# Kernel optimization log

Measured on AMD Instinct MI355X. Metric: run time of the kernel, lower is better.

## Reference

```python
import jax, jax.numpy as jnp
import numpy as np

# Dimensions: state [N, d, n, 2] with last axis = (q, p)
N, D, NN = 256, 8, 32
FEAT = D * NN          # flattened q features = 256
HID = 256              # MLP hidden width
DT = 0.01              # integration step
STEPS = 100            # number of RK4 steps (sequential)


def setup_inputs() -> dict:
    key = jax.random.key(0)
    k0, k1, k2 = jax.random.split(key, 3)
    x0 = 0.1 * jax.random.normal(k0, (N, D, NN, 2), dtype=jnp.float32)
    W1 = jax.random.normal(k1, (FEAT, HID), dtype=jnp.float32) / np.float32(np.sqrt(FEAT))
    b1 = jnp.zeros((HID,), dtype=jnp.float32)
    W2 = jax.random.normal(k2, (HID, 1), dtype=jnp.float32) / np.float32(np.sqrt(HID))
    b2 = jnp.zeros((1,), dtype=jnp.float32)
    return {"x0": x0, "W1": W1, "b1": b1, "W2": W2, "b2": b2}


def _hamiltonian(x, W1, b1, W2, b2):
    # x: [N, d, n, 2] -> H: [N]
    q = x[..., 0]
    p = x[..., 1]
    kinetic = 0.5 * jnp.sum(p * p, axis=(1, 2))          # [N]
    qf = q.reshape(q.shape[0], -1)                        # [N, d*n]
    h = jnp.tanh(qf @ W1 + b1)                            # [N, HID]
    V = (h @ W2 + b2)[:, 0]                               # [N]
    return kinetic + V


def _vector_field(x, params):
    # Hamiltonian vector field: dq/dt = dH/dp, dp/dt = -dH/dq (t-independent)
    g = jax.grad(lambda xx: jnp.sum(_hamiltonian(xx, *params)))(x)  # [N,d,n,2]
    return jnp.stack([g[..., 1], -g[..., 0]], axis=-1)


def _rk4_step(x, eps, params):
    k1 = _vector_field(x, params)
    k2 = _vector_field(x + 0.5 * eps * k1, params)
    k3 = _vector_field(x + 0.5 * eps * k2, params)
    k4 = _vector_field(x + eps * k3, params)
    return x + (eps / 6.0) * (k1 + 2.0 * k2 + 2.0 * k3 + k4)


def reference(x0, W1, b1, W2, b2):
    params = (W1, b1, W2, b2)
    eps = jnp.float32(DT)

    def step(x, _):
        return _rk4_step(x, eps, params), None

    xT, _ = jax.lax.scan(step, x0, None, length=STEPS)
    return xT
```

## Files before the change

kernel.cpp:

```cpp
#include <hip/hip_runtime.h>
#include <stdint.h>


typedef _Float16 v8h __attribute__((ext_vector_type(8)));
typedef float v4f __attribute__((ext_vector_type(4)));

#define NSTEPS 100
#define NEX 25
#define WS 264
#define US 272

#define MFMA_AV(C, A, B) \
    asm("v_mfma_f32_16x16x32_f16 %0, %1, %2, %0" : "+v"(C) : "v"(A), "a"(B))

__device__ __forceinline__ float bfly4(float x) {
    float a = x, b = x;
    asm("v_permlane16_swap_b32 %0, %1" : "+v"(a), "+v"(b));
    float s = a + b;
    float c = s, d = s;
    asm("v_permlane32_swap_b32 %0, %1" : "+v"(c), "+v"(d));
    return c + d;
}

__device__ __forceinline__ float ueval2(float zz, float w4) {
    float e_ = __expf(zz);
    float r_ = __builtin_amdgcn_rcpf(e_ + 1.f);
    return w4 * __builtin_fmaf(-r_, r_, r_);
}

__global__ __launch_bounds__(1024, 4)
void ham_kernel(const float* __restrict__ x0, const float* __restrict__ W1,
                const float* __restrict__ b1, const float* __restrict__ W2,
                float* __restrict__ out)
{
    __shared__ __align__(16)  _Float16 wldsT[256 * WS];
    __shared__ __align__(128) char     upool[20480];
    float*    mscr = (float*)upool;
    _Float16* ubuf = (_Float16*)upool;

    const int t = threadIdx.x;
    const int w = t >> 6;
    const int l = t & 63;
    const int quad = l >> 4;
    const int s = l & 15;
    const int c0 = 16 * w + s;
    const int blk = blockIdx.x;
    const int sel = (s & 3) * US;

    {
        const int c = t & 255;
        const int rbase = (t >> 8) * 64;
        #pragma unroll 1
        for (int r0 = 0; r0 < 64; r0 += 8) {
            v8h h;
            #pragma unroll
            for (int j = 0; j < 8; ++j)
                h[j] = (_Float16)W1[(rbase + r0 + j) * 256 + c];
            *(v8h*)(wldsT + c * WS + rbase + r0) = h;
        }
    }
    __syncthreads();

    v8h wF0[8];
    #pragma unroll
    for (int kk = 0; kk < 8; ++kk)
        wF0[kk] = *(const v8h*)(wldsT + c0 * WS + 32 * kk + 8 * quad);

    v8h wM0[8];
    float* scr0 = mscr + w * 320;
    #pragma unroll
    for (int kb = 0; kb < 16; ++kb) {
        v8h aM[8];
        #pragma unroll
        for (int kk = 0; kk < 8; ++kk)
            aM[kk] = *(const v8h*)(wldsT + (16 * kb + s) * WS
                                          + 32 * kk + 8 * quad);
        v4f D0 = {0.f,0.f,0.f,0.f};
        #pragma unroll
        for (int kk = 0; kk < 8; ++kk)
            D0 = __builtin_amdgcn_mfma_f32_16x16x32_f16(aM[kk], wF0[kk], D0, 0, 0, 0);
        *(v4f*)(scr0 + s * 20 + 4 * quad) = D0;
        asm volatile("s_waitcnt lgkmcnt(0)" ::: "memory");
        if ((quad >> 1) == (kb & 1)) {
            #pragma unroll
            for (int j = 0; j < 8; ++j)
                wM0[kb >> 1][j] = (_Float16)scr0[s * 20 + 8 * (quad & 1) + j];
        }
        asm volatile("s_waitcnt lgkmcnt(0)" ::: "memory");
    }
    __syncthreads();

    const float b1r0 = b1[c0];
    const float w4 = 4.f * W2[c0];
    float2 qp0 = ((const float2*)(x0 + (size_t)blk * 512))[c0];
    const float q0o0 = qp0.x, p0o0 = qp0.y;

    if (quad == 0) {
        ubuf[c0] = (_Float16)q0o0;
        ubuf[US + c0] = (_Float16)p0o0;
        ubuf[2 * US + c0] = (_Float16)0.f;
        ubuf[3 * US + c0] = (_Float16)0.f;
    }
    __syncthreads();
    float z1, P;
    {
        const _Float16* ab = ubuf + sel + 8 * quad;
        v4f C0a = {0.f,0.f,0.f,0.f}, C0b = {0.f,0.f,0.f,0.f};
        #pragma unroll
        for (int kk = 0; kk < 8; kk += 2) {
            v8h a0 = *(const v8h*)(ab + 32 * kk);
            v8h a1 = *(const v8h*)(ab + 32 * (kk + 1));
            C0a = __builtin_amdgcn_mfma_f32_16x16x32_f16(a0, wF0[kk], C0a, 0, 0, 0);
            C0b = __builtin_amdgcn_mfma_f32_16x16x32_f16(a1, wF0[kk + 1], C0b, 0, 0, 0);
        }
        v4f C0s = C0a + C0b;
        z1 = C0s[0] + b1r0;  P = C0s[1];
    }
    __syncthreads();

    const float dt = 0.01f, hdt = 0.005f, dt6 = 0.01f / 6.f;
    const float dtdt6 = dt * dt6, hdt2 = hdt * hdt, dthdt = dt * hdt;
    const float fourdt = 4.f * dt;
    const float qf  = (float)quad;
    const float cPn   = -(qf * 0.25f * dt6);
    const float K2cz1 = 2.f * qf * dt;
    const float K2B   = qf * (4.f - qf) * dtdt6 * 0.25f;
    const float K2Vn  = -(qf * dtdt6 * 0.5f);
    const float K2hdt = 2.f * hdt;
    const float K2hdt2n = -2.f * hdt2;
    const float K2dt  = 2.f * dt;
    const float K2dthdtn = -2.f * dthdt;
    const float wB  = 3.f - qf;

    const int cw = c0 ^ (quad << 3);
    const int R0 = 4 * quad;
    const int wo0 = (R0 + 0) * US + cw;
    const int wo1 = (R0 + 1) * US + (cw ^ 32);
    const int wo2 = (R0 + 2) * US + cw;
    const int wo3 = (R0 + 3) * US + (cw ^ 32);
    const int sx = (s >> 2) & 3;
    const int rbase = s * US + 8 * (quad ^ sx);
    const int sodd = (s & 1) << 5;
    const _Float16* pe = ubuf + rbase + sodd;
    const _Float16* po = ubuf + rbase + 32 - sodd;

    float SBp = 0.f, SVp = 0.f;
    float Y1L = 0.f, Y2L = 0.f;
    float S1p = 0.f, S23p = 0.f;
    float cn = 99.f - qf;

    #pragma unroll 1
    for (int e = 0; e < NEX; ++e) {
        const int bo = (e & 1) * (16 * US);

        float Pp  = __builtin_fmaf(cPn, SBp, P);
        float zp2 = __builtin_fmaf(K2cz1, P, z1 + z1);
        zp2 = __builtin_fmaf(K2B, SBp, zp2);
        zp2 = __builtin_fmaf(K2Vn, SVp, zp2);
        float zb2 = __builtin_fmaf(K2hdt, Pp, zp2);
        float zc2 = __builtin_fmaf(K2hdt2n, Y1L, zb2);
        float zd2 = __builtin_fmaf(K2dt, Pp, zp2);
        zd2 = __builtin_fmaf(K2dthdtn, Y2L, zd2);

        float ua = ueval2(zp2, w4);
        float ub = ueval2(zb2, w4);
        float uc = ueval2(zc2, w4);
        float ud = ueval2(zd2, w4);

        ubuf[bo + wo0] = (_Float16)ua;
        ubuf[bo + wo1] = (_Float16)ub;
        ubuf[bo + wo2] = (_Float16)uc;
        ubuf[bo + wo3] = (_Float16)ud;
        __syncthreads();

        v4f C0s;
        {
            v4f C0a = {0.f,0.f,0.f,0.f}, C0b = {0.f,0.f,0.f,0.f};
            #pragma unroll
            for (int kk = 0; kk < 8; kk += 2) {
                v8h a0 = *(const v8h*)(pe + bo + 32 * kk);
                v8h a1 = *(const v8h*)(po + bo + 32 * kk);
                MFMA_AV(C0a, a0, wM0[kk]);
                MFMA_AV(C0b, a1, wM0[kk + 1]);
            }
            C0s = C0a + C0b;
        }

        float Y1 = C0s[0], Y2 = C0s[1], Y3 = C0s[2], Y4 = C0s[3];
        float tA = Y2 + Y3;
        float A  = Y1 + tA;
        float B  = A + tA + Y4;
        float V  = __builtin_fmaf(wB, B, A);
        float SB = bfly4(B);
        float SV = bfly4(V);

        z1 = __builtin_fmaf(fourdt, P, z1);
        z1 = __builtin_fmaf(-dtdt6, SV, z1);
        P  = __builtin_fmaf(-dt6, SB, P);

        SBp = SB;  SVp = SV;  Y1L = Y1;  Y2L = Y2;

        float tv = ub + uc;
        float sp = __builtin_fmaf(2.f, tv, ua + ud);
        float sq = ua + tv;
        S1p += sp;
        S23p = __builtin_fmaf(cn, sp, S23p) + sq;
        cn -= 4.f;
    }

    const float S1f  = bfly4(S1p);
    const float S23f = bfly4(S23p);
    __syncthreads();
    if (quad == 0) {
        ubuf[c0] = (_Float16)S1f;
        ubuf[US + c0] = (_Float16)S23f;
        ubuf[2 * US + c0] = (_Float16)0.f;
        ubuf[3 * US + c0] = (_Float16)0.f;
    }
    __syncthreads();
    v8h wBt0[8];
    #pragma unroll
    for (int kk = 0; kk < 8; ++kk)
        #pragma unroll
        for (int j = 0; j < 8; ++j)
            wBt0[kk][j] = wldsT[(32 * kk + 8 * quad + j) * WS + c0];
    float D10, D20;
    {
        const _Float16* ab = ubuf + sel + 8 * quad;
        v4f C0a = {0.f,0.f,0.f,0.f}, C0b = {0.f,0.f,0.f,0.f};
        #pragma unroll
        for (int kk = 0; kk < 8; kk += 2) {
            v8h a0 = *(const v8h*)(ab + 32 * kk);
            v8h a1 = *(const v8h*)(ab + 32 * (kk + 1));
            C0a = __builtin_amdgcn_mfma_f32_16x16x32_f16(a0, wBt0[kk], C0a, 0, 0, 0);
            C0b = __builtin_amdgcn_mfma_f32_16x16x32_f16(a1, wBt0[kk + 1], C0b, 0, 0, 0);
        }
        v4f C0s = C0a + C0b;
        D10 = C0s[0];  D20 = C0s[1];
    }
    const float dt6e = 0.01f / 6.f, dtdt6e = 0.01f * dt6e;
    float pT0 = p0o0 - dt6e * D10;
    float qT0 = q0o0 + 0.01f * (float)NSTEPS * p0o0 - dtdt6e * D20;

    if (quad == 0)
        ((float2*)(out + (size_t)blk * 512))[c0] = make_float2(qT0, pT0);
}

extern "C" void kernel_launch(void* const* d_in, const int* in_sizes, int n_in,
                              void* d_out, int out_size, void* d_ws, size_t ws_size,
                              hipStream_t stream) {
    const float* x0 = (const float*)d_in[0];
    const float* W1 = (const float*)d_in[1];
    const float* b1 = (const float*)d_in[2];
    const float* W2 = (const float*)d_in[3];
    float* out = (float*)d_out;
    hipLaunchKernelGGL(ham_kernel, dim3(256), dim3(1024), 0, stream,
                       x0, W1, b1, W2, out);
}
```

Before: 99.79 us.

## Precompute W1 transpose and W1ᵀW1 product in a separate setup kernel

Adds a small setup kernel that writes a half-precision transpose of W1 and the fp16 Gram matrix W1·W1ᵀ into workspace, computed once instead of by each of the 256 blocks. The main kernel then loads its register-resident weight fragments directly from global memory, dropping the 132KB LDS staging buffer, the per-block MFMA Gram computation and several barriers. The backward weight fragments now come from vectorized global loads of W1 issued before the final reduction. The cost is an extra kernel launch and a naive scalar Gram kernel with strided global reads.

```diff
diff --git a/kernel.cpp b/kernel.cpp
--- a/kernel.cpp
+++ b/kernel.cpp
@@ -7,7 +7,6 @@
 
 #define NSTEPS 100
 #define NEX 25
-#define WS 264
 #define US 272
 
 #define MFMA_AV(C, A, B) \
@@ -28,15 +27,30 @@
     return w4 * __builtin_fmaf(-r_, r_, r_);
 }
 
+__global__ __launch_bounds__(256)
+void ham_setup(const float* __restrict__ W1, _Float16* __restrict__ wt,
+               _Float16* __restrict__ mf)
+{
+    const int b = blockIdx.x;
+    const int t = threadIdx.x;
+    wt[b * 256 + t] = (_Float16)W1[t * 256 + b];
+    float acc = 0.f;
+    #pragma unroll 4
+    for (int r = 0; r < 256; ++r) {
+        float wk = (float)(_Float16)W1[r * 256 + b];
+        float wc = (float)(_Float16)W1[r * 256 + t];
+        acc = __builtin_fmaf(wk, wc, acc);
+    }
+    mf[b * 256 + t] = (_Float16)acc;
+}
+
 __global__ __launch_bounds__(1024, 4)
 void ham_kernel(const float* __restrict__ x0, const float* __restrict__ W1,
                 const float* __restrict__ b1, const float* __restrict__ W2,
+                const _Float16* __restrict__ wt, const _Float16* __restrict__ mf,
                 float* __restrict__ out)
 {
-    __shared__ __align__(16)  _Float16 wldsT[256 * WS];
-    __shared__ __align__(128) char     upool[20480];
-    float*    mscr = (float*)upool;
-    _Float16* ubuf = (_Float16*)upool;
+    __shared__ __align__(128) _Float16 ubuf[2 * 16 * US];
 
     const int t = threadIdx.x;
     const int w = t >> 6;
@@ -45,50 +59,15 @@
     const int s = l & 15;
     const int c0 = 16 * w + s;
     const int blk = blockIdx.x;
+    const int kq = 8 * quad;
     const int sel = (s & 3) * US;
 
-    {
-        const int c = t & 255;
-        const int rbase = (t >> 8) * 64;
-        #pragma unroll 1
-        for (int r0 = 0; r0 < 64; r0 += 8) {
-            v8h h;
-            #pragma unroll
-            for (int j = 0; j < 8; ++j)
-                h[j] = (_Float16)W1[(rbase + r0 + j) * 256 + c];
-            *(v8h*)(wldsT + c * WS + rbase + r0) = h;
-        }
-    }
-    __syncthreads();
-
-    v8h wF0[8];
+    v8h wF0[8], wM0[8];
     #pragma unroll
-    for (int kk = 0; kk < 8; ++kk)
-        wF0[kk] = *(const v8h*)(wldsT + c0 * WS + 32 * kk + 8 * quad);
-
-    v8h wM0[8];
-    float* scr0 = mscr + w * 320;
-    #pragma unroll
-    for (int kb = 0; kb < 16; ++kb) {
-        v8h aM[8];
-        #pragma unroll
-        for (int kk = 0; kk < 8; ++kk)
-            aM[kk] = *(const v8h*)(wldsT + (16 * kb + s) * WS
-                                          + 32 * kk + 8 * quad);
-        v4f D0 = {0.f,0.f,0.f,0.f};
-        #pragma unroll
-        for (int kk = 0; kk < 8; ++kk)
-            D0 = __builtin_amdgcn_mfma_f32_16x16x32_f16(aM[kk], wF0[kk], D0, 0, 0, 0);
-        *(v4f*)(scr0 + s * 20 + 4 * quad) = D0;
-        asm volatile("s_waitcnt lgkmcnt(0)" ::: "memory");
-        if ((quad >> 1) == (kb & 1)) {
-            #pragma unroll
-            for (int j = 0; j < 8; ++j)
-                wM0[kb >> 1][j] = (_Float16)scr0[s * 20 + 8 * (quad & 1) + j];
-        }
-        asm volatile("s_waitcnt lgkmcnt(0)" ::: "memory");
-    }
-    __syncthreads();
+    for (int kk = 0; kk < 8; ++kk) {
+        wF0[kk] = *(const v8h*)(wt + c0 * 256 + 32 * kk + kq);
+        wM0[kk] = *(const v8h*)(mf + c0 * 256 + 32 * kk + kq);
+    }
 
     const float b1r0 = b1[c0];
     const float w4 = 4.f * W2[c0];
@@ -208,6 +187,20 @@
         cn -= 4.f;
     }
 
+    v8h wBt0[8];
+    #pragma unroll
+    for (int kk = 0; kk < 8; ++kk) {
+        const float* wp = W1 + c0 * 256 + 32 * kk + kq;
+        v4f lo = *(const v4f*)(wp);
+        v4f hi = *(const v4f*)(wp + 4);
+        v8h h;
+        h[0] = (_Float16)lo[0]; h[1] = (_Float16)lo[1];
+        h[2] = (_Float16)lo[2]; h[3] = (_Float16)lo[3];
+        h[4] = (_Float16)hi[0]; h[5] = (_Float16)hi[1];
+        h[6] = (_Float16)hi[2]; h[7] = (_Float16)hi[3];
+        wBt0[kk] = h;
+    }
+
     const float S1f  = bfly4(S1p);
     const float S23f = bfly4(S23p);
     __syncthreads();
@@ -218,12 +211,6 @@
         ubuf[3 * US + c0] = (_Float16)0.f;
     }
     __syncthreads();
-    v8h wBt0[8];
-    #pragma unroll
-    for (int kk = 0; kk < 8; ++kk)
-        #pragma unroll
-        for (int j = 0; j < 8; ++j)
-            wBt0[kk][j] = wldsT[(32 * kk + 8 * quad + j) * WS + c0];
     float D10, D20;
     {
         const _Float16* ab = ubuf + sel + 8 * quad;
@@ -254,6 +241,9 @@
     const float* b1 = (const float*)d_in[2];
     const float* W2 = (const float*)d_in[3];
     float* out = (float*)d_out;
+    _Float16* wt = (_Float16*)d_ws;
+    _Float16* mf = wt + 256 * 256;
+    hipLaunchKernelGGL(ham_setup, dim3(256), dim3(256), 0, stream, W1, wt, mf);
     hipLaunchKernelGGL(ham_kernel, dim3(256), dim3(1024), 0, stream,
-                       x0, W1, b1, W2, out);
-}
+                       x0, W1, b1, W2, wt, mf, out);
+}
```

After: 109.9 us. 10.2% more time.

## Process eight RK4 steps per synchronized MFMA round instead of four

Applied to the files above, without the earlier changes.

Each loop iteration now covers two RK4 steps per quad (eight per round across quads) by pre-combining the stage terms into two weighted sums per step before the MFMA. The sequential loop drops from 25 rounds to 12, plus a masked tail round for the remaining 4 steps. This halves the number of barrier-separated LDS/MFMA rounds, in exchange for doubling the transcendental work per thread in each round. It also uses a coarser linearization, with the z corrections built from the combined A outputs, which may change accuracy.

```diff
diff --git a/kernel.cpp b/kernel.cpp
--- a/kernel.cpp
+++ b/kernel.cpp
@@ -5,8 +5,7 @@
 typedef _Float16 v8h __attribute__((ext_vector_type(8)));
 typedef float v4f __attribute__((ext_vector_type(4)));
 
-#define NSTEPS 100
-#define NEX 25
+#define NFULL 12
 #define WS 264
 #define US 272
 
@@ -120,17 +119,19 @@
 
     const float dt = 0.01f, hdt = 0.005f, dt6 = 0.01f / 6.f;
     const float dtdt6 = dt * dt6, hdt2 = hdt * hdt, dthdt = dt * hdt;
-    const float fourdt = 4.f * dt;
-    const float qf  = (float)quad;
-    const float cPn   = -(qf * 0.25f * dt6);
-    const float K2cz1 = 2.f * qf * dt;
-    const float K2B   = qf * (4.f - qf) * dtdt6 * 0.25f;
-    const float K2Vn  = -(qf * dtdt6 * 0.5f);
+    const float K8dt = 8.f * dt, K4dt = 4.f * dt;
+    const float j1 = 2.f * (float)quad, j2 = j1 + 1.f;
+    const float cPn1 = -(j1 * 0.125f * dt6), cPn2 = -(j2 * 0.125f * dt6);
+    const float Kz1a = 2.f * j1 * dt,        Kz1b = 2.f * j2 * dt;
+    const float KB1 = dtdt6 * j1 * (8.f - j1) * 0.125f;
+    const float KB2 = dtdt6 * j2 * (8.f - j2) * 0.125f;
+    const float KVn1 = -(j1 * dtdt6 * 0.25f), KVn2 = -(j2 * dtdt6 * 0.25f);
     const float K2hdt = 2.f * hdt;
-    const float K2hdt2n = -2.f * hdt2;
     const float K2dt  = 2.f * dt;
-    const float K2dthdtn = -2.f * dthdt;
-    const float wB  = 3.f - qf;
+    const float KC1n = -(2.f * hdt2) / 3.f;
+    const float KC2n = -(2.f * dthdt) / 3.f;
+    const float w71 = 7.f - j1;
+    const float w31 = 3.f - j1;
 
     const int cw = c0 ^ (quad << 3);
     const int R0 = 4 * quad;
@@ -145,32 +146,48 @@
     const _Float16* po = ubuf + rbase + 32 - sodd;
 
     float SBp = 0.f, SVp = 0.f;
-    float Y1L = 0.f, Y2L = 0.f;
+    float AL1 = 0.f, AL2 = 0.f;
     float S1p = 0.f, S23p = 0.f;
-    float cn = 99.f - qf;
+    float cn1 = 99.f - j1;
 
     #pragma unroll 1
-    for (int e = 0; e < NEX; ++e) {
+    for (int e = 0; e < NFULL; ++e) {
         const int bo = (e & 1) * (16 * US);
 
-        float Pp  = __builtin_fmaf(cPn, SBp, P);
-        float zp2 = __builtin_fmaf(K2cz1, P, z1 + z1);
-        zp2 = __builtin_fmaf(K2B, SBp, zp2);
-        zp2 = __builtin_fmaf(K2Vn, SVp, zp2);
-        float zb2 = __builtin_fmaf(K2hdt, Pp, zp2);
-        float zc2 = __builtin_fmaf(K2hdt2n, Y1L, zb2);
-        float zd2 = __builtin_fmaf(K2dt, Pp, zp2);
-        zd2 = __builtin_fmaf(K2dthdtn, Y2L, zd2);
-
-        float ua = ueval2(zp2, w4);
-        float ub = ueval2(zb2, w4);
-        float uc = ueval2(zc2, w4);
-        float ud = ueval2(zd2, w4);
-
-        ubuf[bo + wo0] = (_Float16)ua;
-        ubuf[bo + wo1] = (_Float16)ub;
-        ubuf[bo + wo2] = (_Float16)uc;
-        ubuf[bo + wo3] = (_Float16)ud;
+        float z1d = z1 + z1;
+        float Pp1  = __builtin_fmaf(cPn1, SBp, P);
+        float zp21 = __builtin_fmaf(Kz1a, P, z1d);
+        zp21 = __builtin_fmaf(KB1, SBp, zp21);
+        zp21 = __builtin_fmaf(KVn1, SVp, zp21);
+        float zb21 = __builtin_fmaf(K2hdt, Pp1, zp21);
+        float zc21 = __builtin_fmaf(KC1n, AL1, zb21);
+        float zd21 = __builtin_fmaf(K2dt, Pp1, zp21);
+        zd21 = __builtin_fmaf(KC2n, AL1, zd21);
+        float Pp2  = __builtin_fmaf(cPn2, SBp, P);
+        float zp22 = __builtin_fmaf(Kz1b, P, z1d);
+        zp22 = __builtin_fmaf(KB2, SBp, zp22);
+        zp22 = __builtin_fmaf(KVn2, SVp, zp22);
+        float zb22 = __builtin_fmaf(K2hdt, Pp2, zp22);
+        float zc22 = __builtin_fmaf(KC1n, AL2, zb22);
+        float zd22 = __builtin_fmaf(K2dt, Pp2, zp22);
+        zd22 = __builtin_fmaf(KC2n, AL2, zd22);
+
+        float ua1 = ueval2(zp21, w4), ub1 = ueval2(zb21, w4);
+        float uc1 = ueval2(zc21, w4), ud1 = ueval2(zd21, w4);
+        float ua2 = ueval2(zp22, w4), ub2 = ueval2(zb22, w4);
+        float uc2 = ueval2(zc22, w4), ud2 = ueval2(zd22, w4);
+
+        float tv1 = ub1 + uc1;
+        float uA1 = ua1 + tv1;
+        float uB1 = __builtin_fmaf(2.f, tv1, ua1 + ud1);
+        float tv2 = ub2 + uc2;
+        float uA2 = ua2 + tv2;
+        float uB2 = __builtin_fmaf(2.f, tv2, ua2 + ud2);
+
+        ubuf[bo + wo0] = (_Float16)uA1;
+        ubuf[bo + wo1] = (_Float16)uB1;
+        ubuf[bo + wo2] = (_Float16)uA2;
+        ubuf[bo + wo3] = (_Float16)uB2;
         __syncthreads();
 
         v4f C0s;
@@ -186,26 +203,85 @@
             C0s = C0a + C0b;
         }
 
-        float Y1 = C0s[0], Y2 = C0s[1], Y3 = C0s[2], Y4 = C0s[3];
-        float tA = Y2 + Y3;
-        float A  = Y1 + tA;
-        float B  = A + tA + Y4;
-        float V  = __builtin_fmaf(wB, B, A);
-        float SB = bfly4(B);
+        float A1 = C0s[0], B1 = C0s[1], A2 = C0s[2], B2 = C0s[3];
+        float Bs = B1 + B2;
+        float V  = __builtin_fmaf(w71, Bs, A1 + A2 - B2);
+        float SB = bfly4(Bs);
         float SV = bfly4(V);
 
-        z1 = __builtin_fmaf(fourdt, P, z1);
+        z1 = __builtin_fmaf(K8dt, P, z1);
         z1 = __builtin_fmaf(-dtdt6, SV, z1);
         P  = __builtin_fmaf(-dt6, SB, P);
 
-        SBp = SB;  SVp = SV;  Y1L = Y1;  Y2L = Y2;
-
-        float tv = ub + uc;
-        float sp = __builtin_fmaf(2.f, tv, ua + ud);
-        float sq = ua + tv;
-        S1p += sp;
-        S23p = __builtin_fmaf(cn, sp, S23p) + sq;
-        cn -= 4.f;
+        SBp = SB;  SVp = SV;  AL1 = A1;  AL2 = A2;
+
+        S1p += uB1 + uB2;
+        S23p = __builtin_fmaf(cn1, uB1, S23p) + uA1;
+        S23p = __builtin_fmaf(cn1 - 1.f, uB2, S23p) + uA2;
+        cn1 -= 8.f;
+    }
+
+    {
+        const float vm = (quad < 2) ? 1.f : 0.f;
+        float z1d = z1 + z1;
+        float Pp1  = __builtin_fmaf(cPn1, SBp, P);
+        float zp21 = __builtin_fmaf(Kz1a, P, z1d);
+        zp21 = __builtin_fmaf(KB1, SBp, zp21);
+        zp21 = __builtin_fmaf(KVn1, SVp, zp21);
+        float zb21 = __builtin_fmaf(K2hdt, Pp1, zp21);
+        float zc21 = __builtin_fmaf(KC1n, AL1, zb21);
+        float zd21 = __builtin_fmaf(K2dt, Pp1, zp21);
+        zd21 = __builtin_fmaf(KC2n, AL1, zd21);
+        float Pp2  = __builtin_fmaf(cPn2, SBp, P);
+        float zp22 = __builtin_fmaf(Kz1b, P, z1d);
+        zp22 = __builtin_fmaf(KB2, SBp, zp22);
+        zp22 = __builtin_fmaf(KVn2, SVp, zp22);
+        float zb22 = __builtin_fmaf(K2hdt, Pp2, zp22);
+        float zc22 = __builtin_fmaf(KC1n, AL2, zb22);
+        float zd22 = __builtin_fmaf(K2dt, Pp2, zp22);
+        zd22 = __builtin_fmaf(KC2n, AL2, zd22);
+
+        float ua1 = ueval2(zp21, w4), ub1 = ueval2(zb21, w4);
+        float uc1 = ueval2(zc21, w4), ud1 = ueval2(zd21, w4);
+        float ua2 = ueval2(zp22, w4), ub2 = ueval2(zb22, w4);
+        float uc2 = ueval2(zc22, w4), ud2 = ueval2(zd22, w4);
+
+        float tv1 = ub1 + uc1;
+        float uA1 = (ua1 + tv1) * vm;
+        float uB1 = __builtin_fmaf(2.f, tv1, ua1 + ud1) * vm;
+        float tv2 = ub2 + uc2;
+        float uA2 = (ua2 + tv2) * vm;
+        float uB2 = __builtin_fmaf(2.f, tv2, ua2 + ud2) * vm;
+
+        ubuf[wo0] = (_Float16)uA1;
+        ubuf[wo1] = (_Float16)uB1;
+        ubuf[wo2] = (_Float16)uA2;
+        ubuf[wo3] = (_Float16)uB2;
+        __syncthreads();
+
+        v4f C0s;
+        {
+            v4f C0a = {0.f,0.f,0.f,0.f}, C0b = {0.f,0.f,0.f,0.f};
+            #pragma unroll
+            for (int kk = 0; kk < 8; kk += 2) {
+                v8h a0 = *(const v8h*)(pe + 32 * kk);
+                v8h a1 = *(const v8h*)(po + 32 * kk);
+                MFMA_AV(C0a, a0, wM0[kk]);
+                MFMA_AV(C0b, a1, wM0[kk + 1]);
+            }
+            C0s = C0a + C0b;
+        }
+        float A1 = C0s[0], B1 = C0s[1], A2 = C0s[2], B2 = C0s[3];
+        float Bs = B1 + B2;
+        float V  = __builtin_fmaf(w31, Bs, A1 + A2 - B2);
+        float SB = bfly4(Bs);
+        float SV = bfly4(V);
+        z1 = __builtin_fmaf(K4dt, P, z1);
+        z1 = __builtin_fmaf(-dtdt6, SV, z1);
+        P  = __builtin_fmaf(-dt6, SB, P);
+        S1p += uB1 + uB2;
+        S23p = __builtin_fmaf(cn1, uB1, S23p) + uA1;
+        S23p = __builtin_fmaf(cn1 - 1.f, uB2, S23p) + uA2;
     }
 
     const float S1f  = bfly4(S1p);
@@ -240,7 +316,7 @@
     }
     const float dt6e = 0.01f / 6.f, dtdt6e = 0.01f * dt6e;
     float pT0 = p0o0 - dt6e * D10;
-    float qT0 = q0o0 + 0.01f * (float)NSTEPS * p0o0 - dtdt6e * D20;
+    float qT0 = q0o0 + 0.01f * 100.f * p0o0 - dtdt6e * D20;
 
     if (quad == 0)
         ((float2*)(out + (size_t)blk * 512))[c0] = make_float2(qT0, pT0);
```

Measured after the change: 92.88 us. -6.9%, faster.
